# Kernel optimization log

Hardware: AMD Instinct MI355X
Metric: run time of the kernel (lower is better)

## Reference

```python
import jax, jax.numpy as jnp
import numpy as np

B, L = 64, 2048
V, E, G = 30, 128, 8          # n_tokens, embedding_size, n_globals
C, F, O = 64, 128, 30         # res_channels, f_channels, n_outputs
K, ND = 2, 9                  # kernel_size, n_dilations
GE = G * E                    # flattened global embedding dim


def causal_conv(x, w, b, dilation):
    # x: [B,Cin,L], w: [Cout,Cin,K] -> [B,Cout,L], causal via left padding
    pad = (w.shape[-1] - 1) * dilation
    out = jax.lax.conv_general_dilated(
        x, w, window_strides=(1,), padding=[(pad, 0)],
        rhs_dilation=(dilation,), dimension_numbers=("NCH", "OIH", "NCH"))
    return out + b[None, :, None]


def setup_inputs() -> dict:
    key = jax.random.key(0)
    ks = jax.random.split(key, 20)
    s = 0.05
    inp = {
        "input_tensor": jax.random.randint(ks[0], (B, L), 0, V),
        "global_input": jax.random.randint(ks[1], (B, G), 0, V),
        "emb_table": jax.random.normal(ks[2], (V, E), jnp.float32) * s,
        "w_causal": jax.random.normal(ks[3], (C, E, K), jnp.float32) * s,
        "b_causal": jnp.zeros((C,), jnp.float32),
        "w_f": jax.random.normal(ks[4], (ND, C, C, K), jnp.float32) * s,
        "b_f": jnp.zeros((ND, C), jnp.float32),
        "w_g": jax.random.normal(ks[5], (ND, C, C, K), jnp.float32) * s,
        "b_g": jnp.zeros((ND, C), jnp.float32),
        "wl_f": jax.random.normal(ks[6], (ND, C, GE), jnp.float32) * s,
        "bl_f": jnp.zeros((ND, C), jnp.float32),
        "wl_g": jax.random.normal(ks[7], (ND, C, GE), jnp.float32) * s,
        "bl_g": jnp.zeros((ND, C), jnp.float32),
        "w_res": jax.random.normal(ks[8], (ND, C, C), jnp.float32) * s,
        "b_res": jnp.zeros((ND, C), jnp.float32),
        "w_fin1": jax.random.normal(ks[9], (F, C), jnp.float32) * s,
        "b_fin1": jnp.zeros((F,), jnp.float32),
        "w_fin2": jax.random.normal(ks[10], (O, F), jnp.float32) * s,
        "b_fin2": jnp.zeros((O,), jnp.float32),
    }
    return inp


def reference(input_tensor, global_input, emb_table, w_causal, b_causal,
              w_f, b_f, w_g, b_g, wl_f, bl_f, wl_g, bl_g,
              w_res, b_res, w_fin1, b_fin1, w_fin2, b_fin2):
    # padding_idx=0: row 0 is zero and receives no gradient
    table = emb_table.at[0].set(0.0)
    emb = table[input_tensor]                     # [B,L,E]
    emb_g = table[global_input].reshape(B, GE)    # [B,G*E]
    x = jnp.transpose(emb, (0, 2, 1))             # [B,E,L]
    res = causal_conv(x, w_causal, b_causal, 1)   # [B,C,L]
    skips = jnp.zeros_like(res)
    for i in range(ND):
        d = 2 ** (i + 1)
        h_f = emb_g @ wl_f[i].T + bl_f[i]         # [B,C]
        h_g = emb_g @ wl_g[i].T + bl_g[i]
        x_f = causal_conv(res, w_f[i], b_f[i], d) + h_f[:, :, None]
        x_g = causal_conv(res, w_g[i], b_g[i], d) + h_g[:, :, None]
        z = jnp.tanh(x_f) * jax.nn.sigmoid(x_g)   # gated activation
        skip = jnp.einsum("oc,bcl->bol", w_res[i], z) + b_res[i][None, :, None]
        res = res + skip
        skips = skips + skip
    out = jax.nn.relu(skips)
    out = jnp.einsum("fc,bcl->bfl", w_fin1, out) + b_fin1[None, :, None]
    out = jax.nn.relu(out)
    out = jnp.einsum("of,bfl->bol", w_fin2, out) + b_fin2[None, :, None]
    return out
```

## Files before the change

kernel.cpp:

```cpp
#include <hip/hip_runtime.h>
#include <stdint.h>

#define Bz 64
#define Lz 2048
#define Vz 30
#define Ez 128
#define Gz 8
#define Cz 64
#define Fz 128
#define Oz 30
#define NDz 9

#define TWOLOG2E 2.8853900817779268f
#define NLOG2E  -1.4426950408889634f

typedef __attribute__((ext_vector_type(8))) short short8;
typedef _Float16 half8 __attribute__((ext_vector_type(8)));
typedef __fp16 fp16x2 __attribute__((ext_vector_type(2)));
typedef __attribute__((ext_vector_type(4))) float floatx4;

#define MFMA16B __builtin_amdgcn_mfma_f32_16x16x32_bf16
#define MFMA16H __builtin_amdgcn_mfma_f32_16x16x32_f16

__device__ __forceinline__ uint16_t f2bf(float f) {
    uint32_t u = __float_as_uint(f);
    u += 0x7fffu + ((u >> 16) & 1u);
    return (uint16_t)(u >> 16);
}
__device__ __forceinline__ uint16_t f2h(float f) {
    return __builtin_bit_cast(uint16_t, (_Float16)f);
}
__device__ __forceinline__ uint32_t pk2h(float lo, float hi) {
    fp16x2 h = __builtin_amdgcn_cvt_pkrtz(lo, hi);
    return __builtin_bit_cast(uint32_t, h);
}
__device__ __forceinline__ uint32_t pkadd(uint32_t oldbits, float a, float b) {
    fp16x2 h = __builtin_bit_cast(fp16x2, oldbits) + __builtin_amdgcn_cvt_pkrtz(a, b);
    return __builtin_bit_cast(uint32_t, h);
}
__device__ __forceinline__ float h2f(uint32_t u16bits) {
    return (float)__builtin_bit_cast(_Float16, (uint16_t)u16bits);
}
__device__ __forceinline__ float fexp2(float x) {
#if __has_builtin(__builtin_amdgcn_exp2f)
    return __builtin_amdgcn_exp2f(x);
#else
    float r; asm("v_exp_f32 %0, %1" : "=v"(r) : "v"(x)); return r;
#endif
}
__device__ __forceinline__ float gatefn(float fl, float gl) {
    float a = fexp2(fl);
    float b = fexp2(gl);
    float ap1 = a + 1.f;
    return (a - 1.f) * __builtin_amdgcn_rcpf(fmaf(ap1, b, ap1));
}

#define N_WB   (NDz * 128 * 128)
#define N_WR   (NDz * 64 * 64)
#define N_W1   (Fz * Cz)
#define N_W2   (32 * Fz)
#define N_PROJ (Vz * Cz)
#define N_WLB  (NDz * 128 * 1024)
#define N_EMB  (Bz * 1024)
#define N_BIAS (NDz * 128)

__global__ void pack_k(const float* __restrict__ w_f, const float* __restrict__ w_g,
                       const float* __restrict__ w_res, const float* __restrict__ w_fin1,
                       const float* __restrict__ w_fin2, const float* __restrict__ w_causal,
                       const float* __restrict__ table, const int* __restrict__ gin,
                       const float* __restrict__ wl_f, const float* __restrict__ wl_g,
                       const float* __restrict__ b_f, const float* __restrict__ b_g,
                       const float* __restrict__ bl_f, const float* __restrict__ bl_g,
                       uint16_t* __restrict__ WB, uint16_t* __restrict__ WrB,
                       uint16_t* __restrict__ W1B, uint16_t* __restrict__ W2B,
                       float* __restrict__ proj0, float* __restrict__ proj1,
                       uint16_t* __restrict__ WLB, uint16_t* __restrict__ embG,
                       float* __restrict__ biasrow) {
    int tid = blockIdx.x * 256 + threadIdx.x;
    if (tid < N_WB) {
        int i = tid >> 14, rem = tid & 16383, ch = rem >> 7, k = rem & 127;
        int kin = k & 63, tap = (k < 64) ? 1 : 0;
        float v = (ch < 64) ? w_f[((i * Cz + ch) * Cz + kin) * 2 + tap] * TWOLOG2E
                            : w_g[((i * Cz + (ch - 64)) * Cz + kin) * 2 + tap] * NLOG2E;
        WB[tid] = f2h(v);
        return;
    }
    tid -= N_WB;
    if (tid < N_WR) { WrB[tid] = f2h(w_res[tid]); return; }
    tid -= N_WR;
    if (tid < N_W1) { W1B[tid] = f2h(w_fin1[tid]); return; }
    tid -= N_W1;
    if (tid < N_W2) {
        int o = tid >> 7, f = tid & 127;
        W2B[tid] = f2h(o < Oz ? w_fin2[o * Fz + f] : 0.f);
        return;
    }
    tid -= N_W2;
    if (tid < N_PROJ) {
        int v = tid >> 6, c = tid & 63;
        float s0 = 0.f, s1 = 0.f;
        if (v != 0) {
            for (int e = 0; e < Ez; e++) {
                float tv = table[v * Ez + e];
                s0 += w_causal[(c * Ez + e) * 2 + 0] * tv;
                s1 += w_causal[(c * Ez + e) * 2 + 1] * tv;
            }
        }
        proj0[tid] = s0; proj1[tid] = s1;
        return;
    }
    tid -= N_PROJ;
    if (tid < N_WLB) {
        int row = tid >> 10, j = tid & 1023;
        int i = row >> 7, rem = row & 127, fg = rem >> 6, c = rem & 63;
        const float* wl = fg ? wl_g : wl_f;
        float sc = fg ? NLOG2E : TWOLOG2E;
        WLB[tid] = f2bf(wl[((size_t)(i * Cz + c)) * 1024 + j] * sc);
        return;
    }
    tid -= N_WLB;
    if (tid < N_EMB) {
        int b = tid >> 10, j = tid & 1023;
        int g = j >> 7, e = j & 127;
        int v = gin[b * Gz + g];
        embG[tid] = f2bf(v ? table[v * Ez + e] : 0.f);
        return;
    }
    tid -= N_EMB;
    if (tid < N_BIAS) {
        int i = tid >> 7, rem = tid & 127, fg = rem >> 6, c = rem & 63;
        float bsum = (fg ? b_g : b_f)[i * Cz + c] + (fg ? bl_g : bl_f)[i * Cz + c];
        biasrow[tid] = bsum * (fg ? NLOG2E : TWOLOG2E);
    }
}

__global__ __launch_bounds__(256) void hgemm_k(
    const uint16_t* __restrict__ WLB, const uint16_t* __restrict__ embG,
    const float* __restrict__ biasrow, float* __restrict__ hhT) {
    __shared__ float red[4][4][64][4];
    int tx = threadIdx.x, lane = tx & 63, wave = tx >> 6;
    int nl = lane & 15, quad = lane >> 4;
    int row0 = blockIdx.x * 16;
    floatx4 acc[4];
#pragma unroll
    for (int nt = 0; nt < 4; nt++)
#pragma unroll
        for (int r = 0; r < 4; r++) acc[nt][r] = 0.f;
    const uint16_t* ap = WLB + (size_t)(row0 + nl) * 1024 + quad * 8;
#pragma unroll
    for (int k8 = 0; k8 < 8; k8++) {
        int ks = wave * 8 + k8;
        short8 a = *(const short8*)(ap + ks * 32);
#pragma unroll
        for (int nt = 0; nt < 4; nt++) {
            short8 bb = *(const short8*)(embG + (size_t)(nt * 16 + nl) * 1024 + ks * 32 + quad * 8);
            acc[nt] = MFMA16B(a, bb, acc[nt], 0, 0, 0);
        }
    }
#pragma unroll
    for (int nt = 0; nt < 4; nt++)
#pragma unroll
        for (int r = 0; r < 4; r++) red[nt][wave][lane][r] = acc[nt][r];
    __syncthreads();
    {
        int nt = wave;
#pragma unroll
        for (int r = 0; r < 4; r++) {
            float s = red[nt][0][lane][r] + red[nt][1][lane][r] +
                      red[nt][2][lane][r] + red[nt][3][lane][r];
            hhT[(size_t)(row0 + quad * 4 + r) * 64 + nt * 16 + nl] =
                s + biasrow[row0 + quad * 4 + r];
        }
    }
}

__global__ __launch_bounds__(256) void init_k(
    const int* __restrict__ tok, const float* __restrict__ b_causal,
    const float* __restrict__ proj0, const float* __restrict__ proj1,
    uint16_t* __restrict__ res) {
    int tx = threadIdx.x;
    int q = tx & 15, tl = tx >> 4;
    int b = blockIdx.y;
    int t = blockIdx.x * 16 + tl;
    int v1 = tok[b * Lz + t];
    int v0 = (t > 0) ? tok[b * Lz + t - 1] : 0;
    float4 p1 = ((const float4*)(proj1 + v1 * Cz))[q];
    float4 p0 = ((const float4*)(proj0 + v0 * Cz))[q];
    float4 bc = ((const float4*)b_causal)[q];
    float rx = p1.x + p0.x + bc.x, ry = p1.y + p0.y + bc.y;
    float rz = p1.z + p0.z + bc.z, rw = p1.w + p0.w + bc.w;
    *(uint2*)(res + ((size_t)(b * Lz + t)) * Cz + q * 4) =
        make_uint2(pk2h(rx, ry), pk2h(rz, rw));
}

__global__ __launch_bounds__(256, 3) void fused_k(
    const uint16_t* __restrict__ rin, uint16_t* __restrict__ rout,
    const uint16_t* __restrict__ WB, const uint16_t* __restrict__ WrB,
    const float* __restrict__ hhT, const float* __restrict__ b_res) {
    __shared__ __align__(16) uint16_t R[192 * 72];
    __shared__ __align__(16) uint16_t Zb[192 * 64];
    int tx = threadIdx.x;
    int lane = tx & 63, wave = tx >> 6;
    int nl = lane & 15, quad = lane >> 4;
    int b = blockIdx.y, t0 = blockIdx.x * 128;
    const uint16_t* rb16 = rin + ((size_t)b * Lz) * Cz;

    if (t0 != 0) {
        const uint16_t* src = rb16 + (size_t)(t0 - 64) * Cz;
#pragma unroll
        for (int it = 0; it < 6; it++) {
            int id = it * 256 + tx, row = id >> 3, c8 = id & 7;
            uint4 v = *(const uint4*)(src + (size_t)row * Cz + c8 * 8);
            *(uint4*)(R + row * 72 + c8 * 8) = v;
        }
    } else {
#pragma unroll
        for (int it = 0; it < 6; it++) {
            int id = it * 256 + tx, row = id >> 3, c8 = id & 7;
            int t = row - 64;
            uint4 v = make_uint4(0u, 0u, 0u, 0u);
            if (t >= 0) v = *(const uint4*)(rb16 + (size_t)t * Cz + c8 * 8);
            *(uint4*)(R + row * 72 + c8 * 8) = v;
        }
    }
    floatx4 ss[8];
#pragma unroll
    for (int j = 0; j < 8; j++)
#pragma unroll
        for (int r = 0; r < 4; r++) ss[j][r] = 0.f;
    __syncthreads();

    const int chq = wave * 16 + quad * 4;
    const int zmask = (nl & 7) << 3;
    const int zwr  = chq ^ zmask;
    const int zrd0 = (quad * 8) ^ zmask;
    const int zrd1 = (quad * 8 + 32) ^ zmask;
    const int NT0[5] = {0, 0, 1, 2, 4};

#pragma unroll
    for (int l = 0; l < 5; l++) {
        const int d = 2 << l;
        const int nt0 = NT0[l];
        const uint16_t* wf = WB + l * 16384 + (wave * 16 + nl) * 128 + quad * 8;
        half8 AF[4], AG[4];
#pragma unroll
        for (int ks = 0; ks < 4; ks++) {
            AF[ks] = *(const half8*)(wf + ks * 32);
            AG[ks] = *(const half8*)(wf + 64 * 128 + ks * 32);
        }
        const uint16_t* wr = WrB + l * 4096 + (wave * 16 + nl) * 64 + quad * 8;
        half8 AR0 = *(const half8*)(wr);
        half8 AR1 = *(const half8*)(wr + 32);
        float hfv[4], hgv[4], brv[4];
        const float* hp = hhT + ((size_t)(l * 128 + wave * 16 + quad * 4)) * 64 + b;
#pragma unroll
        for (int r = 0; r < 4; r++) { hfv[r] = hp[r * 64]; hgv[r] = hp[4096 + r * 64]; }
        const float* brp = b_res + l * Cz + wave * 16 + quad * 4;
#pragma unroll
        for (int r = 0; r < 4; r++) brv[r] = brp[r];

#pragma unroll
        for (int nt = 0; nt < 12; nt++) {
            if (nt < nt0) continue;
            int rowa = nt * 16 + nl;
            int rowb = rowa - d;
            if (nt * 16 < d) rowb = rowb < 0 ? 0 : rowb;
            const uint16_t* ra = R + rowa * 72 + quad * 8;
            const uint16_t* rb = R + rowb * 72 + quad * 8;
            half8 b0 = *(const half8*)(ra);
            half8 b1 = *(const half8*)(ra + 32);
            half8 b2 = *(const half8*)(rb);
            half8 b3 = *(const half8*)(rb + 32);
            floatx4 aF, aG;
#pragma unroll
            for (int r = 0; r < 4; r++) { aF[r] = hfv[r]; aG[r] = hgv[r]; }
            aF = MFMA16H(AF[0], b0, aF, 0, 0, 0); aG = MFMA16H(AG[0], b0, aG, 0, 0, 0);
            aF = MFMA16H(AF[1], b1, aF, 0, 0, 0); aG = MFMA16H(AG[1], b1, aG, 0, 0, 0);
            aF = MFMA16H(AF[2], b2, aF, 0, 0, 0); aG = MFMA16H(AG[2], b2, aG, 0, 0, 0);
            aF = MFMA16H(AF[3], b3, aF, 0, 0, 0); aG = MFMA16H(AG[3], b3, aG, 0, 0, 0);
            float z0 = gatefn(aF[0], aG[0]);
            float z1 = gatefn(aF[1], aG[1]);
            float z2 = gatefn(aF[2], aG[2]);
            float z3 = gatefn(aF[3], aG[3]);
            *(uint2*)(Zb + rowa * 64 + zwr) = make_uint2(pk2h(z0, z1), pk2h(z2, z3));
        }
        __syncthreads();

        if (t0 != 0) {
#pragma unroll
            for (int nt = 0; nt < 12; nt++) {
                if (nt < nt0) continue;
                int pos = nt * 16 + nl;
                const uint16_t* zb0 = Zb + pos * 64;
                floatx4 a2;
#pragma unroll
                for (int r = 0; r < 4; r++) a2[r] = brv[r];
                a2 = MFMA16H(AR0, *(const half8*)(zb0 + zrd0), a2, 0, 0, 0);
                a2 = MFMA16H(AR1, *(const half8*)(zb0 + zrd1), a2, 0, 0, 0);
                uint16_t* rp = R + pos * 72 + chq;
                uint2 oldp = *(uint2*)rp;
                *(uint2*)rp = make_uint2(pkadd(oldp.x, a2[0], a2[1]),
                                         pkadd(oldp.y, a2[2], a2[3]));
                if (nt >= 4) {
#pragma unroll
                    for (int r = 0; r < 4; r++) ss[nt - 4][r] += a2[r];
                }
            }
        } else {
#pragma unroll
            for (int nt = 0; nt < 12; nt++) {
                if (nt < nt0) continue;
                int pos = nt * 16 + nl;
                const uint16_t* zb0 = Zb + pos * 64;
                floatx4 a2;
#pragma unroll
                for (int r = 0; r < 4; r++) a2[r] = brv[r];
                a2 = MFMA16H(AR0, *(const half8*)(zb0 + zrd0), a2, 0, 0, 0);
                a2 = MFMA16H(AR1, *(const half8*)(zb0 + zrd1), a2, 0, 0, 0);
                bool ok = (pos >= 64);
                uint16_t* rp = R + pos * 72 + chq;
                uint2 oldp = *(uint2*)rp;
                uint32_t ux = ok ? pkadd(oldp.x, a2[0], a2[1]) : 0u;
                uint32_t uy = ok ? pkadd(oldp.y, a2[2], a2[3]) : 0u;
                *(uint2*)rp = make_uint2(ux, uy);
                if (nt >= 4) {
#pragma unroll
                    for (int r = 0; r < 4; r++) ss[nt - 4][r] += a2[r];
                }
            }
        }
        __syncthreads();
    }

    uint16_t* ro = rout + ((size_t)b * Lz) * Cz;
#pragma unroll
    for (int j = 0; j < 8; j++) {
        size_t off = (size_t)(t0 + j * 16 + nl) * Cz + chq;
        uint2 rv = *(const uint2*)(rb16 + off);
        *(uint2*)(ro + off) = make_uint2(pkadd(rv.x, ss[j][0], ss[j][1]),
                                         pkadd(rv.y, ss[j][2], ss[j][3]));
    }
}

__global__ __launch_bounds__(256, 4) void layer_k(
    const uint16_t* __restrict__ rin, uint16_t* __restrict__ rout,
    const uint16_t* __restrict__ WBl, const uint16_t* __restrict__ WrBl,
    const float* __restrict__ hhT, const float* __restrict__ b_res,
    int i, int d) {
    __shared__ __align__(16) uint16_t X[64 * 136];
    __shared__ __align__(16) uint16_t Z[64 * 72];
    int tx = threadIdx.x;
    int lane = tx & 63, wave = tx >> 6;
    int nl = lane & 15, quad = lane >> 4;
    int b = blockIdx.y, t0 = blockIdx.x * 64;
    const uint16_t* rb16 = rin + ((size_t)b * Lz) * Cz;

#pragma unroll
    for (int it = 0; it < 2; it++) {
        int id = it * 256 + tx, row = id >> 3, c8 = id & 7;
        uint4 v = *(const uint4*)(rb16 + (size_t)(t0 + row) * Cz + c8 * 8);
        *(uint4*)(X + row * 136 + c8 * 8) = v;
    }
#pragma unroll
    for (int it = 0; it < 2; it++) {
        int id = it * 256 + tx, row = id >> 3, c8 = id & 7;
        int tb = t0 + row - d;
        uint4 v = make_uint4(0u, 0u, 0u, 0u);
        if (tb >= 0) v = *(const uint4*)(rb16 + (size_t)tb * Cz + c8 * 8);
        *(uint4*)(X + row * 136 + 64 + c8 * 8) = v;
    }

    half8 AF[4], AG[4], AR[2];
    {
        const uint16_t* wf = WBl + (wave * 16 + nl) * 128 + quad * 8;
#pragma unroll
        for (int ks = 0; ks < 4; ks++) {
            AF[ks] = *(const half8*)(wf + ks * 32);
            AG[ks] = *(const half8*)(wf + 64 * 128 + ks * 32);
        }
        const uint16_t* wr = WrBl + (wave * 16 + nl) * 64 + quad * 8;
#pragma unroll
        for (int ks = 0; ks < 2; ks++) AR[ks] = *(const half8*)(wr + ks * 32);
    }
    float hfv[4], hgv[4], brv[4];
    {
        const float* hp = hhT + ((size_t)(i * 128 + wave * 16 + quad * 4)) * 64 + b;
#pragma unroll
        for (int r = 0; r < 4; r++) {
            hfv[r] = hp[r * 64];
            hgv[r] = hp[4096 + r * 64];
        }
        const float* brp = b_res + i * Cz + wave * 16 + quad * 4;
#pragma unroll
        for (int r = 0; r < 4; r++) brv[r] = brp[r];
    }
    __syncthreads();

    floatx4 accF[4], accG[4];
#pragma unroll
    for (int nt = 0; nt < 4; nt++)
#pragma unroll
        for (int r = 0; r < 4; r++) { accF[nt][r] = hfv[r]; accG[nt][r] = hgv[r]; }
#pragma unroll
    for (int nt = 0; nt < 4; nt++) {
        const uint16_t* xp = X + (nt * 16 + nl) * 136 + quad * 8;
#pragma unroll
        for (int ks = 0; ks < 4; ks++) {
            half8 bf = *(const half8*)(xp + ks * 32);
            accF[nt] = MFMA16H(AF[ks], bf, accF[nt], 0, 0, 0);
            accG[nt] = MFMA16H(AG[ks], bf, accG[nt], 0, 0, 0);
        }
    }

    int chq = wave * 16 + quad * 4;
#pragma unroll
    for (int nt = 0; nt < 4; nt++) {
        int pos = nt * 16 + nl;
        float z0 = gatefn(accF[nt][0], accG[nt][0]);
        float z1 = gatefn(accF[nt][1], accG[nt][1]);
        float z2 = gatefn(accF[nt][2], accG[nt][2]);
        float z3 = gatefn(accF[nt][3], accG[nt][3]);
        *(uint2*)(Z + pos * 72 + chq) = make_uint2(pk2h(z0, z1), pk2h(z2, z3));
    }
    __syncthreads();

    floatx4 acc2[4];
#pragma unroll
    for (int nt = 0; nt < 4; nt++)
#pragma unroll
        for (int r = 0; r < 4; r++) acc2[nt][r] = brv[r];
#pragma unroll
    for (int nt = 0; nt < 4; nt++) {
        const uint16_t* zp = Z + (nt * 16 + nl) * 72 + quad * 8;
        acc2[nt] = MFMA16H(AR[0], *(const half8*)zp, acc2[nt], 0, 0, 0);
        acc2[nt] = MFMA16H(AR[1], *(const half8*)(zp + 32), acc2[nt], 0, 0, 0);
    }

    uint16_t* ro = rout + ((size_t)b * Lz) * Cz;
#pragma unroll
    for (int nt = 0; nt < 4; nt++) {
        size_t off = (size_t)(t0 + nt * 16 + nl) * Cz + chq;
        uint2 rv = *(const uint2*)(rb16 + off);
        *(uint2*)(ro + off) = make_uint2(pkadd(rv.x, acc2[nt][0], acc2[nt][1]),
                                         pkadd(rv.y, acc2[nt][2], acc2[nt][3]));
    }
}

__global__ __launch_bounds__(256, 3) void final_k(
    const uint16_t* __restrict__ res0, const uint16_t* __restrict__ resF,
    const uint16_t* __restrict__ W1B, const uint16_t* __restrict__ W2B,
    const float* __restrict__ b_fin1, const float* __restrict__ b_fin2,
    float* __restrict__ out) {
    __shared__ __align__(16) uint16_t S[128 * 72];
    __shared__ __align__(16) uint16_t Mi[128 * 136];
    int tx = threadIdx.x;
    int lane = tx & 63, wave = tx >> 6;
    int nl = lane & 15, quad = lane >> 4;
    int b = blockIdx.y, t0 = blockIdx.x * 128;
    const uint16_t* r0 = res0 + ((size_t)b * Lz) * Cz;
    const uint16_t* rF = resF + ((size_t)b * Lz) * Cz;

    half8 A1[2][2], A2[2][4];
#pragma unroll
    for (int mt = 0; mt < 2; mt++) {
        const uint16_t* w1 = W1B + (wave * 32 + mt * 16 + nl) * 64 + quad * 8;
#pragma unroll
        for (int ks = 0; ks < 2; ks++) A1[mt][ks] = *(const half8*)(w1 + ks * 32);
        const uint16_t* w2 = W2B + (mt * 16 + nl) * 128 + quad * 8;
#pragma unroll
        for (int ks = 0; ks < 4; ks++) A2[mt][ks] = *(const half8*)(w2 + ks * 32);
    }
#pragma unroll
    for (int it = 0; it < 4; it++) {
        int id = it * 256 + tx, row = id >> 3, c8 = id & 7;
        uint4 fv = *(const uint4*)(rF + (size_t)(t0 + row) * Cz + c8 * 8);
        uint4 ov = *(const uint4*)(r0 + (size_t)(t0 + row) * Cz + c8 * 8);
        float s0 = fmaxf(h2f(fv.x) - h2f(ov.x), 0.f);
        float s1 = fmaxf(h2f(fv.x >> 16) - h2f(ov.x >> 16), 0.f);
        float s2 = fmaxf(h2f(fv.y) - h2f(ov.y), 0.f);
        float s3 = fmaxf(h2f(fv.y >> 16) - h2f(ov.y >> 16), 0.f);
        float s4 = fmaxf(h2f(fv.z) - h2f(ov.z), 0.f);
        float s5 = fmaxf(h2f(fv.z >> 16) - h2f(ov.z >> 16), 0.f);
        float s6 = fmaxf(h2f(fv.w) - h2f(ov.w), 0.f);
        float s7 = fmaxf(h2f(fv.w >> 16) - h2f(ov.w >> 16), 0.f);
        *(uint4*)(S + row * 72 + c8 * 8) =
            make_uint4(pk2h(s0, s1), pk2h(s2, s3), pk2h(s4, s5), pk2h(s6, s7));
    }
    __syncthreads();

    floatx4 accM[2][8];
    float b1v[2][4];
#pragma unroll
    for (int mt = 0; mt < 2; mt++)
#pragma unroll
        for (int r = 0; r < 4; r++) b1v[mt][r] = b_fin1[wave * 32 + mt * 16 + quad * 4 + r];
#pragma unroll
    for (int mt = 0; mt < 2; mt++)
#pragma unroll
        for (int nt = 0; nt < 8; nt++)
#pragma unroll
            for (int r = 0; r < 4; r++) accM[mt][nt][r] = b1v[mt][r];
#pragma unroll
    for (int nt = 0; nt < 8; nt++) {
        const uint16_t* sp = S + (nt * 16 + nl) * 72 + quad * 8;
#pragma unroll
        for (int ks = 0; ks < 2; ks++) {
            half8 s = *(const half8*)(sp + ks * 32);
            accM[0][nt] = MFMA16H(A1[0][ks], s, accM[0][nt], 0, 0, 0);
            accM[1][nt] = MFMA16H(A1[1][ks], s, accM[1][nt], 0, 0, 0);
        }
    }
#pragma unroll
    for (int mt = 0; mt < 2; mt++)
#pragma unroll
        for (int nt = 0; nt < 8; nt++) {
            int pos = nt * 16 + nl;
            int fq = wave * 32 + mt * 16 + quad * 4;
            float m0 = fmaxf(accM[mt][nt][0], 0.f), m1 = fmaxf(accM[mt][nt][1], 0.f);
            float m2 = fmaxf(accM[mt][nt][2], 0.f), m3 = fmaxf(accM[mt][nt][3], 0.f);
            *(uint2*)(Mi + pos * 136 + fq) = make_uint2(pk2h(m0, m1), pk2h(m2, m3));
        }
    __syncthreads();

    floatx4 accO[2][2];
#pragma unroll
    for (int mt = 0; mt < 2; mt++)
#pragma unroll
        for (int r = 0; r < 4; r++) {
            int o = mt * 16 + quad * 4 + r;
            float bo = (o < Oz) ? b_fin2[o] : 0.f;
            accO[mt][0][r] = bo; accO[mt][1][r] = bo;
        }
#pragma unroll
    for (int ntl = 0; ntl < 2; ntl++) {
        int nt = wave * 2 + ntl;
        const uint16_t* mp = Mi + (nt * 16 + nl) * 136 + quad * 8;
#pragma unroll
        for (int ks = 0; ks < 4; ks++) {
            half8 m = *(const half8*)(mp + ks * 32);
            accO[0][ntl] = MFMA16H(A2[0][ks], m, accO[0][ntl], 0, 0, 0);
            accO[1][ntl] = MFMA16H(A2[1][ks], m, accO[1][ntl], 0, 0, 0);
        }
    }
#pragma unroll
    for (int mt = 0; mt < 2; mt++)
#pragma unroll
        for (int ntl = 0; ntl < 2; ntl++)
#pragma unroll
            for (int r = 0; r < 4; r++) {
                int o = mt * 16 + quad * 4 + r;
                if (o < Oz)
                    out[((size_t)b * Oz + o) * Lz + t0 + (wave * 2 + ntl) * 16 + nl] =
                        accO[mt][ntl][r];
            }
}

extern "C" void kernel_launch(void* const* d_in, const int* in_sizes, int n_in,
                              void* d_out, int out_size, void* d_ws, size_t ws_size,
                              hipStream_t stream) {
    const int*   tok      = (const int*)d_in[0];
    const int*   gin      = (const int*)d_in[1];
    const float* table    = (const float*)d_in[2];
    const float* w_causal = (const float*)d_in[3];
    const float* b_causal = (const float*)d_in[4];
    const float* w_f      = (const float*)d_in[5];
    const float* b_f      = (const float*)d_in[6];
    const float* w_g      = (const float*)d_in[7];
    const float* b_g      = (const float*)d_in[8];
    const float* wl_f     = (const float*)d_in[9];
    const float* bl_f     = (const float*)d_in[10];
    const float* wl_g     = (const float*)d_in[11];
    const float* bl_g     = (const float*)d_in[12];
    const float* w_res    = (const float*)d_in[13];
    const float* b_res    = (const float*)d_in[14];
    const float* w_fin1   = (const float*)d_in[15];
    const float* b_fin1   = (const float*)d_in[16];
    const float* w_fin2   = (const float*)d_in[17];
    const float* b_fin2   = (const float*)d_in[18];
    float* out = (float*)d_out;

    const size_t NRES = (size_t)Bz * Lz * Cz;
    uint16_t* u16 = (uint16_t*)d_ws;
    uint16_t* resA = u16;
    uint16_t* resB = resA + NRES;
    uint16_t* resC = resB + NRES;
    uint16_t* WB   = resC + NRES;
    uint16_t* WrB  = WB + N_WB;
    uint16_t* W1B  = WrB + N_WR;
    uint16_t* W2B  = W1B + N_W1;
    uint16_t* WLB  = W2B + N_W2;
    uint16_t* embG = WLB + N_WLB;
    float* hhT     = (float*)(embG + N_EMB);
    float* proj0   = hhT + 73728;
    float* proj1   = proj0 + N_PROJ;
    float* biasrow = proj1 + N_PROJ;

    int npack = N_WB + N_WR + N_W1 + N_W2 + N_PROJ + N_WLB + N_EMB + N_BIAS;
    pack_k<<<(npack + 255) / 256, 256, 0, stream>>>(
        w_f, w_g, w_res, w_fin1, w_fin2, w_causal, table, gin,
        wl_f, wl_g, b_f, b_g, bl_f, bl_g,
        WB, WrB, W1B, W2B, proj0, proj1, WLB, embG, biasrow);
    hgemm_k<<<72, 256, 0, stream>>>(WLB, embG, biasrow, hhT);
    init_k<<<dim3(Lz / 16, Bz), 256, 0, stream>>>(tok, b_causal, proj0, proj1, resA);

    fused_k<<<dim3(Lz / 128, Bz), 256, 0, stream>>>(resA, resB, WB, WrB, hhT, b_res);
    layer_k<<<dim3(Lz / 64, Bz), 256, 0, stream>>>(
        resB, resC, WB + (size_t)5 * 16384, WrB + (size_t)5 * 4096, hhT, b_res, 5, 64);
    layer_k<<<dim3(Lz / 64, Bz), 256, 0, stream>>>(
        resC, resB, WB + (size_t)6 * 16384, WrB + (size_t)6 * 4096, hhT, b_res, 6, 128);
    layer_k<<<dim3(Lz / 64, Bz), 256, 0, stream>>>(
        resB, resC, WB + (size_t)7 * 16384, WrB + (size_t)7 * 4096, hhT, b_res, 7, 256);
    layer_k<<<dim3(Lz / 64, Bz), 256, 0, stream>>>(
        resC, resB, WB + (size_t)8 * 16384, WrB + (size_t)8 * 4096, hhT, b_res, 8, 512);
    final_k<<<dim3(Lz / 128, Bz), 256, 0, stream>>>(resA, resB, W1B, W2B,
                                                    b_fin1, b_fin2, out);
}
```

Measured before the change: 272.0 us.

## Fuse dilation layers 5 and 6 into one kernel with halo recompute

Adds pair_k, which loads a 128-step tile plus a 192-step causal halo of the residual into shared memory and runs layers 5 and 6 back to back there. Layer 5 is recomputed over the halo rows that layer 6 needs, so the residual no longer makes a global round trip between the two layers and one launch is removed. In exchange, the kernel does extra MFMA work on the halo and uses much more shared memory, which lowers occupancy (launch bounds of 2). The buffer ping-pong for the remaining layer_k calls and for final_k is rewired to match.

Result: faster. 262.9 us (-3.3%).

```diff
diff --git a/kernel.cpp b/kernel.cpp
--- a/kernel.cpp
+++ b/kernel.cpp
@@ -339,6 +339,121 @@
         uint2 rv = *(const uint2*)(rb16 + off);
         *(uint2*)(ro + off) = make_uint2(pkadd(rv.x, ss[j][0], ss[j][1]),
                                          pkadd(rv.y, ss[j][2], ss[j][3]));
+    }
+}
+
+__global__ __launch_bounds__(256, 2) void pair_k(
+    const uint16_t* __restrict__ rin, uint16_t* __restrict__ rout,
+    const uint16_t* __restrict__ WB, const uint16_t* __restrict__ WrB,
+    const float* __restrict__ hhT, const float* __restrict__ b_res) {
+    __shared__ __align__(16) uint16_t R[320 * 72];
+    __shared__ __align__(16) uint16_t Zb[256 * 64];
+    int tx = threadIdx.x;
+    int lane = tx & 63, wave = tx >> 6;
+    int nl = lane & 15, quad = lane >> 4;
+    int b = blockIdx.y, t0 = blockIdx.x * 128;
+    const uint16_t* rb16 = rin + ((size_t)b * Lz) * Cz;
+
+    if (t0 >= 192) {
+        const uint16_t* src = rb16 + (size_t)(t0 - 192) * Cz;
+#pragma unroll
+        for (int it = 0; it < 10; it++) {
+            int id = it * 256 + tx, row = id >> 3, c8 = id & 7;
+            uint4 v = *(const uint4*)(src + (size_t)row * Cz + c8 * 8);
+            *(uint4*)(R + row * 72 + c8 * 8) = v;
+        }
+    } else {
+#pragma unroll
+        for (int it = 0; it < 10; it++) {
+            int id = it * 256 + tx, row = id >> 3, c8 = id & 7;
+            int t = t0 - 192 + row;
+            uint4 v = make_uint4(0u, 0u, 0u, 0u);
+            if (t >= 0) v = *(const uint4*)(rb16 + (size_t)t * Cz + c8 * 8);
+            *(uint4*)(R + row * 72 + c8 * 8) = v;
+        }
+    }
+    __syncthreads();
+
+    const int chq = wave * 16 + quad * 4;
+    const int zmask = (nl & 7) << 3;
+    const int zwr  = chq ^ zmask;
+    const int zrd0 = (quad * 8) ^ zmask;
+    const int zrd1 = (quad * 8 + 32) ^ zmask;
+    const int thr = 192 - t0;
+
+#pragma unroll
+    for (int li = 0; li < 2; li++) {
+        const int l = 5 + li;
+        const int d = 64 << li;
+        const int ntLo = li ? 12 : 4;
+        const uint16_t* wf = WB + l * 16384 + (wave * 16 + nl) * 128 + quad * 8;
+        half8 AF[4], AG[4];
+#pragma unroll
+        for (int ks = 0; ks < 4; ks++) {
+            AF[ks] = *(const half8*)(wf + ks * 32);
+            AG[ks] = *(const half8*)(wf + 64 * 128 + ks * 32);
+        }
+        const uint16_t* wr = WrB + l * 4096 + (wave * 16 + nl) * 64 + quad * 8;
+        half8 AR0 = *(const half8*)(wr);
+        half8 AR1 = *(const half8*)(wr + 32);
+        float hfv[4], hgv[4], brv[4];
+        const float* hp = hhT + ((size_t)(l * 128 + wave * 16 + quad * 4)) * 64 + b;
+#pragma unroll
+        for (int r = 0; r < 4; r++) { hfv[r] = hp[r * 64]; hgv[r] = hp[4096 + r * 64]; }
+        const float* brp = b_res + l * Cz + wave * 16 + quad * 4;
+#pragma unroll
+        for (int r = 0; r < 4; r++) brv[r] = brp[r];
+
+#pragma unroll
+        for (int nt = ntLo; nt < 20; nt++) {
+            if (li == 0 && nt * 16 < thr) continue;
+            int rowa = nt * 16 + nl;
+            int rowb = rowa - d;
+            const uint16_t* ra = R + rowa * 72 + quad * 8;
+            const uint16_t* rb = R + rowb * 72 + quad * 8;
+            half8 b0 = *(const half8*)(ra);
+            half8 b1 = *(const half8*)(ra + 32);
+            half8 b2 = *(const half8*)(rb);
+            half8 b3 = *(const half8*)(rb + 32);
+            floatx4 aF, aG;
+#pragma unroll
+            for (int r = 0; r < 4; r++) { aF[r] = hfv[r]; aG[r] = hgv[r]; }
+            aF = MFMA16H(AF[0], b0, aF, 0, 0, 0); aG = MFMA16H(AG[0], b0, aG, 0, 0, 0);
+            aF = MFMA16H(AF[1], b1, aF, 0, 0, 0); aG = MFMA16H(AG[1], b1, aG, 0, 0, 0);
+            aF = MFMA16H(AF[2], b2, aF, 0, 0, 0); aG = MFMA16H(AG[2], b2, aG, 0, 0, 0);
+            aF = MFMA16H(AF[3], b3, aF, 0, 0, 0); aG = MFMA16H(AG[3], b3, aG, 0, 0, 0);
+            float z0 = gatefn(aF[0], aG[0]);
+            float z1 = gatefn(aF[1], aG[1]);
+            float z2 = gatefn(aF[2], aG[2]);
+            float z3 = gatefn(aF[3], aG[3]);
+            *(uint2*)(Zb + (rowa - 64) * 64 + zwr) = make_uint2(pk2h(z0, z1), pk2h(z2, z3));
+        }
+        __syncthreads();
+
+#pragma unroll
+        for (int nt = ntLo; nt < 20; nt++) {
+            if (li == 0 && nt * 16 < thr) continue;
+            int pos = nt * 16 + nl;
+            const uint16_t* zb0 = Zb + (pos - 64) * 64;
+            floatx4 a2;
+#pragma unroll
+            for (int r = 0; r < 4; r++) a2[r] = brv[r];
+            a2 = MFMA16H(AR0, *(const half8*)(zb0 + zrd0), a2, 0, 0, 0);
+            a2 = MFMA16H(AR1, *(const half8*)(zb0 + zrd1), a2, 0, 0, 0);
+            uint16_t* rp = R + pos * 72 + chq;
+            uint2 oldp = *(uint2*)rp;
+            *(uint2*)rp = make_uint2(pkadd(oldp.x, a2[0], a2[1]),
+                                     pkadd(oldp.y, a2[2], a2[3]));
+        }
+        __syncthreads();
+    }
+
+    uint16_t* ro = rout + ((size_t)b * Lz) * Cz;
+#pragma unroll
+    for (int j = 0; j < 8; j++) {
+        int s = 192 + j * 16 + nl;
+        size_t off = (size_t)(t0 + j * 16 + nl) * Cz + chq;
+        *(uint2*)(ro + off) = *(const uint2*)(R + s * 72 + chq);
     }
 }
 
@@ -604,14 +719,11 @@
     init_k<<<dim3(Lz / 16, Bz), 256, 0, stream>>>(tok, b_causal, proj0, proj1, resA);
 
     fused_k<<<dim3(Lz / 128, Bz), 256, 0, stream>>>(resA, resB, WB, WrB, hhT, b_res);
+    pair_k<<<dim3(Lz / 128, Bz), 256, 0, stream>>>(resB, resC, WB, WrB, hhT, b_res);
     layer_k<<<dim3(Lz / 64, Bz), 256, 0, stream>>>(
-        resB, resC, WB + (size_t)5 * 16384, WrB + (size_t)5 * 4096, hhT, b_res, 5, 64);
+        resC, resB, WB + (size_t)7 * 16384, WrB + (size_t)7 * 4096, hhT, b_res, 7, 256);
     layer_k<<<dim3(Lz / 64, Bz), 256, 0, stream>>>(
-        resC, resB, WB + (size_t)6 * 16384, WrB + (size_t)6 * 4096, hhT, b_res, 6, 128);
-    layer_k<<<dim3(Lz / 64, Bz), 256, 0, stream>>>(
-        resB, resC, WB + (size_t)7 * 16384, WrB + (size_t)7 * 4096, hhT, b_res, 7, 256);
-    layer_k<<<dim3(Lz / 64, Bz), 256, 0, stream>>>(
-        resC, resB, WB + (size_t)8 * 16384, WrB + (size_t)8 * 4096, hhT, b_res, 8, 512);
-    final_k<<<dim3(Lz / 128, Bz), 256, 0, stream>>>(resA, resB, W1B, W2B,
+        resB, resC, WB + (size_t)8 * 16384, WrB + (size_t)8 * 4096, hhT, b_res, 8, 512);
+    final_k<<<dim3(Lz / 128, Bz), 256, 0, stream>>>(resA, resC, W1B, W2B,
                                                     b_fin1, b_fin2, out);
 }
```
